# Kernel tuning notes

Hardware: AMD Instinct MI355X
Metric: run time of the kernel (lower is better)

Reference implementation:

```python
import jax, jax.numpy as jnp
import numpy as np

EPS = 0.01

def _hos_pool(x):
    # x: [B, C, T] -> [B, 4C]; matches torch mean/std(unbiased)/skew/kurt over time
    T = x.shape[-1]
    mean = jnp.mean(x, axis=-1)                              # [B, C]
    centered = x - mean[..., None]                           # [B, C, T]
    var_b = jnp.sum(centered * centered, axis=-1) / (T - 1)  # unbiased variance
    std = jnp.sqrt(var_b)
    norm = centered / jnp.maximum(std, EPS)[..., None]
    n2 = norm * norm
    skew = jnp.mean(n2 * norm, axis=-1)
    kurt = jnp.mean(n2 * n2, axis=-1)
    return jnp.concatenate([mean, std, skew, kurt], axis=-1)  # [B, 4C]


def setup_inputs() -> dict:
    key = jax.random.key(0)
    ks = jax.random.split(key, 6)
    B, C, T, BR = 32, 512, 4000, 2
    sc = 1.0 / np.sqrt(4 * C)
    return {
        "x_a": jax.random.normal(ks[0], (B, C, T), dtype=jnp.float32),
        "x_b": jax.random.normal(ks[1], (B, C, T), dtype=jnp.float32),
        "W1": jax.random.normal(ks[2], (C, 4 * C), dtype=jnp.float32) * sc,
        "b1": jax.random.normal(ks[3], (C,), dtype=jnp.float32) * sc,
        "W2": jax.random.normal(ks[4], (BR, C, C), dtype=jnp.float32) * (1.0 / np.sqrt(C)),
        "b2": jax.random.normal(ks[5], (BR, C), dtype=jnp.float32) * (1.0 / np.sqrt(C)),
    }


def reference(x_a, x_b, W1, b1, W2, b2):
    # f: [B, 2, C, T]
    f = jnp.stack([x_a, x_b], axis=1)
    x_sum = x_a + x_b                                        # [B, C, T]
    stats = _hos_pool(x_sum)                                 # [B, 4C]
    h = stats @ W1.T + b1                                    # [B, C_hidden]
    # per-branch gate logits: [B, BR, C]
    s = jnp.einsum("bh,koh->bko", h, W2) + b2[None, :, :]
    s = jax.nn.softmax(s, axis=1)[..., None]                 # [B, BR, C, 1]
    return jnp.sum(f * s, axis=1)                            # [B, C, T]
```

## Files before the change

### kernel.cpp

```cpp
#include <hip/hip_runtime.h>
#include <hip/hip_bf16.h>
#include <math.h>

#define T_LEN 4000
#define T4    1000
#define BDIM  256
#define EPS   0.01f

__device__ __forceinline__ float waveReduceSum(float v) {
    #pragma unroll
    for (int off = 32; off > 0; off >>= 1) v += __shfl_down(v, off, 64);
    return v;
}

__global__ __launch_bounds__(BDIM) void stats_kernel(
    const float* __restrict__ xa, const float* __restrict__ xb,
    float* __restrict__ stats, int C) {
    __shared__ float red[4][4];

    const int r = blockIdx.x;
    const int b = r / C;
    const int c = r - b * C;
    const int tid = threadIdx.x;
    const int wave = tid >> 6, lane = tid & 63;

    const float4* a4 = (const float4*)(xa + (size_t)r * T_LEN);
    const float4* b4 = (const float4*)(xb + (size_t)r * T_LEN);

    float s1 = 0.f, s2 = 0.f, s3 = 0.f, s4 = 0.f;
    for (int i = tid; i < T4; i += BDIM) {
        float4 av = a4[i], bv = b4[i];
        float x0 = av.x + bv.x, x1 = av.y + bv.y, x2 = av.z + bv.z, x3 = av.w + bv.w;
        float q0 = x0 * x0, q1 = x1 * x1, q2 = x2 * x2, q3 = x3 * x3;
        s1 += (x0 + x1) + (x2 + x3);
        s2 += (q0 + q1) + (q2 + q3);
        s3 += (q0 * x0 + q1 * x1) + (q2 * x2 + q3 * x3);
        s4 += (q0 * q0 + q1 * q1) + (q2 * q2 + q3 * q3);
    }
    s1 = waveReduceSum(s1);
    s2 = waveReduceSum(s2);
    s3 = waveReduceSum(s3);
    s4 = waveReduceSum(s4);
    if (lane == 0) { red[wave][0] = s1; red[wave][1] = s2; red[wave][2] = s3; red[wave][3] = s4; }
    __syncthreads();

    if (tid == 0) {
        float S1 = red[0][0] + red[1][0] + red[2][0] + red[3][0];
        float S2 = red[0][1] + red[1][1] + red[2][1] + red[3][1];
        float S3 = red[0][2] + red[1][2] + red[2][2] + red[3][2];
        float S4 = red[0][3] + red[1][3] + red[2][3] + red[3][3];
        const float invT = 1.0f / T_LEN;
        float mean = S1 * invT;
        float m = mean, m2c = m * m;
        float M2 = S2 - S1 * m;
        float M3 = S3 - 3.0f * m * S2 + 2.0f * m2c * S1;
        float M4 = S4 - 4.0f * m * S3 + 6.0f * m2c * S2 - 3.0f * m2c * m * S1;
        float var_b = M2 / (float)(T_LEN - 1);
        float sd = sqrtf(fmaxf(var_b, 0.0f));
        float d = fmaxf(sd, EPS);
        float inv = 1.0f / d;
        float inv2 = inv * inv;
        float skew = (M3 * invT) * inv2 * inv;
        float kurt = (M4 * invT) * inv2 * inv2;
        float* srow = stats + (size_t)b * (4 * C);
        srow[c]         = mean;
        srow[C + c]     = sd;
        srow[2 * C + c] = skew;
        srow[3 * C + c] = kurt;
    }
}

__global__ __launch_bounds__(BDIM) void h_kernel(
    const float* __restrict__ stats, const float* __restrict__ W1,
    const float* __restrict__ b1, float* __restrict__ h, int C) {
    __shared__ float sst[2048];
    const int H = 4 * C;
    const int groups = C / 4;
    const int b = blockIdx.x / groups;
    const int grp = blockIdx.x - b * groups;
    const int tid = threadIdx.x;
    const int wave = tid >> 6, lane = tid & 63;
    const int o = grp * 4 + wave;

    for (int i = tid; i < H; i += BDIM) sst[i] = stats[(size_t)b * H + i];
    __syncthreads();

    const float4* s4 = (const float4*)sst;
    const float4* w4 = (const float4*)(W1 + (size_t)o * H);
    float acc = 0.f;
    const int n4 = H / 4;
    #pragma unroll
    for (int it = 0; it < 8; ++it) {
        int idx = it * 64 + lane;
        if (idx < n4) {
            float4 w = w4[idx];
            float4 s = s4[idx];
            acc += (w.x * s.x + w.y * s.y) + (w.z * s.z + w.w * s.w);
        }
    }
    acc = waveReduceSum(acc);
    if (lane == 0) h[(size_t)b * C + o] = acc + b1[o];
}

__global__ __launch_bounds__(BDIM) void mixgate_kernel(
    const float* __restrict__ xa, const float* __restrict__ xb,
    const float* __restrict__ h, const float* __restrict__ W2,
    const float* __restrict__ b2, float* __restrict__ out, int C) {
    __shared__ float red0[4], red1[4];
    __shared__ float sg;

    const int r = blockIdx.x;
    const int b = r / C;
    const int c = r - b * C;
    const int tid = threadIdx.x;
    const int wave = tid >> 6, lane = tid & 63;

    const float2* h2 = (const float2*)(h + (size_t)b * C);
    const float2* w0 = (const float2*)(W2 + (size_t)c * C);
    const float2* w1 = (const float2*)(W2 + (size_t)C * C + (size_t)c * C);
    float l0 = 0.f, l1 = 0.f;
    for (int i = tid; i < C / 2; i += BDIM) {
        float2 hv = h2[i];
        float2 a0 = w0[i];
        float2 a1 = w1[i];
        l0 += hv.x * a0.x + hv.y * a0.y;
        l1 += hv.x * a1.x + hv.y * a1.y;
    }
    l0 = waveReduceSum(l0);
    l1 = waveReduceSum(l1);
    if (lane == 0) { red0[wave] = l0; red1[wave] = l1; }
    __syncthreads();
    if (tid == 0) {
        float L0 = (red0[0] + red0[1]) + (red0[2] + red0[3]) + b2[c];
        float L1 = (red1[0] + red1[1]) + (red1[2] + red1[3]) + b2[C + c];
        sg = 1.0f / (1.0f + expf(L1 - L0));
    }
    __syncthreads();

    const float g = sg;
    const float hg = 1.0f - g;

    const float4* a4 = (const float4*)(xa + (size_t)r * T_LEN);
    const float4* b4 = (const float4*)(xb + (size_t)r * T_LEN);
    float4* o4 = (float4*)(out + (size_t)r * T_LEN);
    for (int i = tid; i < T4; i += BDIM) {
        float4 a = a4[i], bb = b4[i];
        o4[i] = make_float4(g * a.x + hg * bb.x,
                            g * a.y + hg * bb.y,
                            g * a.z + hg * bb.z,
                            g * a.w + hg * bb.w);
    }
}

extern "C" void kernel_launch(void* const* d_in, const int* in_sizes, int n_in,
                              void* d_out, int out_size, void* d_ws, size_t ws_size,
                              hipStream_t stream) {
    const float* xa = (const float*)d_in[0];
    const float* xb = (const float*)d_in[1];
    const float* W1 = (const float*)d_in[2];
    const float* b1 = (const float*)d_in[3];
    const float* W2 = (const float*)d_in[4];
    const float* b2 = (const float*)d_in[5];
    float* out = (float*)d_out;

    const int C = in_sizes[3];
    const int B = in_sizes[0] / (C * T_LEN);

    float* stats = (float*)d_ws;
    float* h     = stats + (size_t)B * 4 * C;

    stats_kernel<<<B * C, BDIM, 0, stream>>>(xa, xb, stats, C);
    h_kernel<<<B * (C / 4), BDIM, 0, stream>>>(stats, W1, b1, h, C);
    mixgate_kernel<<<B * C, BDIM, 0, stream>>>(xa, xb, h, W2, b2, out, C);
}
```

Before: 692.4 us.

## Split gate GEMV from blend, unroll streaming loads, reverse blend order

Moves the per-row gate computation out of the blend kernel into a separate gate_kernel that handles four channels per block. The blend kernel then only streams xa and xb. It issues all loads up front, uses nontemporal loads and stores, and walks rows in reverse so the rows the stats pass touched last may still be in cache. The stats kernel is also unrolled to issue all its loads at once. This adds one kernel launch, and it hard-codes the T_LEN/BDIM unroll structure along with C values up to 512.

Result: no change. 681.4 us (-1.6%).

```diff
diff --git a/kernel.cpp b/kernel.cpp
--- a/kernel.cpp
+++ b/kernel.cpp
@@ -1,5 +1,4 @@
 #include <hip/hip_runtime.h>
-#include <hip/hip_bf16.h>
 #include <math.h>
 
 #define T_LEN 4000
@@ -7,6 +6,8 @@
 #define BDIM  256
 #define EPS   0.01f
 
+typedef float v4f __attribute__((ext_vector_type(4)));
+
 __device__ __forceinline__ float waveReduceSum(float v) {
     #pragma unroll
     for (int off = 32; off > 0; off >>= 1) v += __shfl_down(v, off, 64);
@@ -24,19 +25,37 @@
     const int tid = threadIdx.x;
     const int wave = tid >> 6, lane = tid & 63;
 
-    const float4* a4 = (const float4*)(xa + (size_t)r * T_LEN);
-    const float4* b4 = (const float4*)(xb + (size_t)r * T_LEN);
+    const v4f* a4 = (const v4f*)(xa + (size_t)r * T_LEN);
+    const v4f* b4 = (const v4f*)(xb + (size_t)r * T_LEN);
+
+    const bool has4 = (tid < (T4 - 3 * BDIM));
+    v4f av0 = a4[tid];
+    v4f bv0 = b4[tid];
+    v4f av1 = a4[tid + BDIM];
+    v4f bv1 = b4[tid + BDIM];
+    v4f av2 = a4[tid + 2 * BDIM];
+    v4f bv2 = b4[tid + 2 * BDIM];
+    v4f av3 = {0.f, 0.f, 0.f, 0.f};
+    v4f bv3 = {0.f, 0.f, 0.f, 0.f};
+    if (has4) { av3 = a4[tid + 3 * BDIM]; bv3 = b4[tid + 3 * BDIM]; }
 
     float s1 = 0.f, s2 = 0.f, s3 = 0.f, s4 = 0.f;
-    for (int i = tid; i < T4; i += BDIM) {
-        float4 av = a4[i], bv = b4[i];
-        float x0 = av.x + bv.x, x1 = av.y + bv.y, x2 = av.z + bv.z, x3 = av.w + bv.w;
-        float q0 = x0 * x0, q1 = x1 * x1, q2 = x2 * x2, q3 = x3 * x3;
-        s1 += (x0 + x1) + (x2 + x3);
-        s2 += (q0 + q1) + (q2 + q3);
-        s3 += (q0 * x0 + q1 * x1) + (q2 * x2 + q3 * x3);
-        s4 += (q0 * q0 + q1 * q1) + (q2 * q2 + q3 * q3);
-    }
+    #define ACC(av, bv)                                                      \
+    {                                                                        \
+        float x0 = av.x + bv.x, x1 = av.y + bv.y,                            \
+              x2 = av.z + bv.z, x3 = av.w + bv.w;                            \
+        float q0 = x0 * x0, q1 = x1 * x1, q2 = x2 * x2, q3 = x3 * x3;        \
+        s1 += (x0 + x1) + (x2 + x3);                                         \
+        s2 += (q0 + q1) + (q2 + q3);                                         \
+        s3 += (q0 * x0 + q1 * x1) + (q2 * x2 + q3 * x3);                     \
+        s4 += (q0 * q0 + q1 * q1) + (q2 * q2 + q3 * q3);                     \
+    }
+    ACC(av0, bv0)
+    ACC(av1, bv1)
+    ACC(av2, bv2)
+    ACC(av3, bv3)
+    #undef ACC
+
     s1 = waveReduceSum(s1);
     s2 = waveReduceSum(s2);
     s3 = waveReduceSum(s3);
@@ -73,7 +92,7 @@
 __global__ __launch_bounds__(BDIM) void h_kernel(
     const float* __restrict__ stats, const float* __restrict__ W1,
     const float* __restrict__ b1, float* __restrict__ h, int C) {
-    __shared__ float sst[2048];
+    __shared__ __align__(16) float sst[2048];
     const int H = 4 * C;
     const int groups = C / 4;
     const int b = blockIdx.x / groups;
@@ -82,73 +101,97 @@
     const int wave = tid >> 6, lane = tid & 63;
     const int o = grp * 4 + wave;
 
-    for (int i = tid; i < H; i += BDIM) sst[i] = stats[(size_t)b * H + i];
+    const v4f* src4 = (const v4f*)(stats + (size_t)b * H);
+    v4f* sst4 = (v4f*)sst;
+    for (int i = tid; i < H / 4; i += BDIM) sst4[i] = src4[i];
     __syncthreads();
 
-    const float4* s4 = (const float4*)sst;
-    const float4* w4 = (const float4*)(W1 + (size_t)o * H);
+    const v4f* s4 = (const v4f*)sst;
+    const v4f* w4 = (const v4f*)(W1 + (size_t)o * H);
     float acc = 0.f;
-    const int n4 = H / 4;
     #pragma unroll
     for (int it = 0; it < 8; ++it) {
         int idx = it * 64 + lane;
-        if (idx < n4) {
-            float4 w = w4[idx];
-            float4 s = s4[idx];
-            acc += (w.x * s.x + w.y * s.y) + (w.z * s.z + w.w * s.w);
-        }
+        v4f w = w4[idx];
+        v4f s = s4[idx];
+        acc += (w.x * s.x + w.y * s.y) + (w.z * s.z + w.w * s.w);
     }
     acc = waveReduceSum(acc);
     if (lane == 0) h[(size_t)b * C + o] = acc + b1[o];
 }
 
-__global__ __launch_bounds__(BDIM) void mixgate_kernel(
-    const float* __restrict__ xa, const float* __restrict__ xb,
+__global__ __launch_bounds__(BDIM) void gate_kernel(
     const float* __restrict__ h, const float* __restrict__ W2,
-    const float* __restrict__ b2, float* __restrict__ out, int C) {
-    __shared__ float red0[4], red1[4];
-    __shared__ float sg;
-
-    const int r = blockIdx.x;
-    const int b = r / C;
-    const int c = r - b * C;
+    const float* __restrict__ b2, float* __restrict__ g, int C) {
+    __shared__ __align__(16) float hs[512];
+    const int groups = C / 4;
+    const int b  = blockIdx.x / groups;
+    const int cg = blockIdx.x - b * groups;
     const int tid = threadIdx.x;
     const int wave = tid >> 6, lane = tid & 63;
-
-    const float2* h2 = (const float2*)(h + (size_t)b * C);
-    const float2* w0 = (const float2*)(W2 + (size_t)c * C);
-    const float2* w1 = (const float2*)(W2 + (size_t)C * C + (size_t)c * C);
+    const int c = cg * 4 + wave;
+
+    for (int i = tid; i < C; i += BDIM) hs[i] = h[(size_t)b * C + i];
+    __syncthreads();
+
+    const v4f* h4 = (const v4f*)hs;
+    const v4f* w0 = (const v4f*)(W2 + (size_t)c * C);
+    const v4f* w1 = (const v4f*)(W2 + (size_t)C * C + (size_t)c * C);
     float l0 = 0.f, l1 = 0.f;
-    for (int i = tid; i < C / 2; i += BDIM) {
-        float2 hv = h2[i];
-        float2 a0 = w0[i];
-        float2 a1 = w1[i];
-        l0 += hv.x * a0.x + hv.y * a0.y;
-        l1 += hv.x * a1.x + hv.y * a1.y;
+    #pragma unroll
+    for (int it = 0; it < 2; ++it) {
+        int i = it * 64 + lane;
+        v4f hv = h4[i];
+        v4f a0 = w0[i];
+        v4f a1 = w1[i];
+        l0 += (hv.x * a0.x + hv.y * a0.y) + (hv.z * a0.z + hv.w * a0.w);
+        l1 += (hv.x * a1.x + hv.y * a1.y) + (hv.z * a1.z + hv.w * a1.w);
     }
     l0 = waveReduceSum(l0);
     l1 = waveReduceSum(l1);
-    if (lane == 0) { red0[wave] = l0; red1[wave] = l1; }
-    __syncthreads();
-    if (tid == 0) {
-        float L0 = (red0[0] + red0[1]) + (red0[2] + red0[3]) + b2[c];
-        float L1 = (red1[0] + red1[1]) + (red1[2] + red1[3]) + b2[C + c];
-        sg = 1.0f / (1.0f + expf(L1 - L0));
-    }
-    __syncthreads();
-
-    const float g = sg;
-    const float hg = 1.0f - g;
-
-    const float4* a4 = (const float4*)(xa + (size_t)r * T_LEN);
-    const float4* b4 = (const float4*)(xb + (size_t)r * T_LEN);
-    float4* o4 = (float4*)(out + (size_t)r * T_LEN);
-    for (int i = tid; i < T4; i += BDIM) {
-        float4 a = a4[i], bb = b4[i];
-        o4[i] = make_float4(g * a.x + hg * bb.x,
-                            g * a.y + hg * bb.y,
-                            g * a.z + hg * bb.z,
-                            g * a.w + hg * bb.w);
+    if (lane == 0) {
+        float L0 = l0 + b2[c];
+        float L1 = l1 + b2[C + c];
+        g[(size_t)b * C + c] = 1.0f / (1.0f + expf(L1 - L0));
+    }
+}
+
+__global__ __launch_bounds__(BDIM) void blend_kernel(
+    const float* __restrict__ xa, const float* __restrict__ xb,
+    const float* __restrict__ g, float* __restrict__ out) {
+    const int r = (int)gridDim.x - 1 - (int)blockIdx.x;
+    const int tid = threadIdx.x;
+
+    const v4f* a4 = (const v4f*)(xa + (size_t)r * T_LEN);
+    const v4f* b4 = (const v4f*)(xb + (size_t)r * T_LEN);
+    v4f* o4 = (v4f*)(out + (size_t)r * T_LEN);
+
+    const bool has4 = (tid < (T4 - 3 * BDIM));
+    v4f A0 = __builtin_nontemporal_load(a4 + tid);
+    v4f B0 = __builtin_nontemporal_load(b4 + tid);
+    v4f A1 = __builtin_nontemporal_load(a4 + tid + BDIM);
+    v4f B1 = __builtin_nontemporal_load(b4 + tid + BDIM);
+    v4f A2 = __builtin_nontemporal_load(a4 + tid + 2 * BDIM);
+    v4f B2 = __builtin_nontemporal_load(b4 + tid + 2 * BDIM);
+    v4f A3 = {0.f, 0.f, 0.f, 0.f};
+    v4f B3 = {0.f, 0.f, 0.f, 0.f};
+    if (has4) {
+        A3 = __builtin_nontemporal_load(a4 + tid + 3 * BDIM);
+        B3 = __builtin_nontemporal_load(b4 + tid + 3 * BDIM);
+    }
+
+    const float gv = g[r];
+    const float hg = 1.0f - gv;
+
+    v4f O0 = A0 * gv + B0 * hg;
+    v4f O1 = A1 * gv + B1 * hg;
+    v4f O2 = A2 * gv + B2 * hg;
+    __builtin_nontemporal_store(O0, o4 + tid);
+    __builtin_nontemporal_store(O1, o4 + tid + BDIM);
+    __builtin_nontemporal_store(O2, o4 + tid + 2 * BDIM);
+    if (has4) {
+        v4f O3 = A3 * gv + B3 * hg;
+        __builtin_nontemporal_store(O3, o4 + tid + 3 * BDIM);
     }
 }
 
@@ -168,8 +211,10 @@
 
     float* stats = (float*)d_ws;
     float* h     = stats + (size_t)B * 4 * C;
+    float* g     = stats;
 
     stats_kernel<<<B * C, BDIM, 0, stream>>>(xa, xb, stats, C);
     h_kernel<<<B * (C / 4), BDIM, 0, stream>>>(stats, W1, b1, h, C);
-    mixgate_kernel<<<B * C, BDIM, 0, stream>>>(xa, xb, h, W2, b2, out, C);
-}
+    gate_kernel<<<B * (C / 4), BDIM, 0, stream>>>(h, W2, b2, g, C);
+    blend_kernel<<<B * C, BDIM, 0, stream>>>(xa, xb, g, out);
+}
```
